# Kernel tuning notes

Measured on AMD Instinct MI355X. Metric: run time of the kernel, lower is better.

## Reference

```python
import jax, jax.numpy as jnp
import numpy as np

N, E, D, LM, NF, M = 512, 16384, 1280, 1024, 256, 64

def setup_inputs() -> dict:
    key = jax.random.key(0)
    ks = jax.random.split(key, 10)
    lm_embedding = jax.random.normal(ks[0], (1, N + 2, LM), jnp.float32)
    node_feat = jax.random.normal(ks[1], (N, NF), jnp.float32)
    edge_feat = jax.random.uniform(ks[2], (E, 1), jnp.float32)
    src = jax.random.randint(ks[3], (E,), 0, N)
    dst = jax.random.randint(ks[4], (E,), 0, N)
    mask_index = jax.random.randint(ks[5], (M,), 0, N)
    W_g = jax.random.normal(ks[6], (D, D), jnp.float32) / np.sqrt(D).astype(np.float32)
    b_g = jnp.zeros((D,), jnp.float32)
    W_d = jax.random.normal(ks[7], (D, 1), jnp.float32) / np.sqrt(D).astype(np.float32)
    b_d = jnp.zeros((1,), jnp.float32)
    W_m = jax.random.normal(ks[8], (D, 2), jnp.float32) / np.sqrt(D).astype(np.float32)
    b_m = jnp.zeros((2,), jnp.float32)
    return {"lm_embedding": lm_embedding, "node_feat": node_feat, "edge_feat": edge_feat,
            "src": src, "dst": dst, "mask_index": mask_index,
            "W_g": W_g, "b_g": b_g, "W_d": W_d, "b_d": b_d, "W_m": W_m, "b_m": b_m}

def reference(lm_embedding, node_feat, edge_feat, src, dst, mask_index,
              W_g, b_g, W_d, b_d, W_m, b_m):
    # concat LM embedding (strip BOS/EOS) with structural features -> (N, D)
    h = jnp.concatenate([lm_embedding[0, 1:-1, :], node_feat], axis=1)
    # GINConv('max'): messages = h[src] * edge_weight, max-reduce onto dst
    msg = h[src] * edge_feat                                   # (E, D)
    neigh = jax.ops.segment_max(msg, dst, num_segments=h.shape[0])
    neigh = jnp.where(jnp.isneginf(neigh), 0.0, neigh)         # isolated nodes -> 0 (DGL semantics)
    rst = (h + neigh) @ W_g + b_g                              # (1+eps)*h + neigh, eps=0, then Linear
    node_output = rst + h                                      # residual
    # dis_pred[i, j] = sigmoid(W_d . (h_j - h_i) + b_d); collapse to per-node projection
    p = (node_output @ W_d)[:, 0]                              # (N,)
    dis_pred = jax.nn.sigmoid(p[None, :] - p[:, None] + b_d[0])[..., None]  # (N, N, 1)
    mask_pred = jnp.tanh(node_output[mask_index] @ W_m + b_m)  # (M, 2)
    return (dis_pred, mask_pred)
```

## Files before the change

### kernel.cpp

```cpp
#include <hip/hip_runtime.h>
#include <float.h>
#include <math.h>

#define N 512
#define E 16384
#define D 1280
#define LMDIM 1024
#define NFDIM 256
#define M 64
#define MAXDEG 512

#define WPROJ_BLOCKS 161
#define BIN_BLOCKS 32

__device__ __forceinline__ float4 h_vec4(const float* __restrict__ lm,
                                         const float* __restrict__ nf,
                                         int i, int t) {
  return (t < 256) ? *(const float4*)&lm[(size_t)(i + 1) * LMDIM + t * 4]
                   : *(const float4*)&nf[(size_t)i * NFDIM + (t - 256) * 4];
}

__device__ __forceinline__ float wred(float v) {
#pragma unroll
  for (int off = 32; off > 0; off >>= 1) v += __shfl_xor(v, off, 64);
  return v;
}

__global__ __launch_bounds__(512) void prep_kernel(
    const float* __restrict__ Wg, const float* __restrict__ Wd,
    const float* __restrict__ Wm, const float* __restrict__ bg,
    const int* __restrict__ src, const int* __restrict__ dst,
    const float* __restrict__ ew,
    float* __restrict__ wd2, float* __restrict__ wm2,
    float* __restrict__ consts,
    int* __restrict__ cnt, int2* __restrict__ bin) {
  const int b = blockIdx.x;
  const int t = threadIdx.x;
  if (b < WPROJ_BLOCKS) {
    const int wid = t >> 6, lane = t & 63;
    const int r = b * 8 + wid;
    if (r > D) return;
    const float* row = (r < D) ? &Wg[(size_t)r * D] : bg;
    float d0 = 0.f, d1 = 0.f, d2 = 0.f;
#pragma unroll
    for (int k = 0; k < 5; ++k) {
      int u = lane + 64 * k;
      float4 wv = *(const float4*)&row[u * 4];
      float4 vd = *(const float4*)&Wd[u * 4];
      d0 += wv.x * vd.x + wv.y * vd.y + wv.z * vd.z + wv.w * vd.w;
      float4 m01 = *(const float4*)&Wm[u * 8];
      float4 m23 = *(const float4*)&Wm[u * 8 + 4];
      d1 += wv.x * m01.x + wv.y * m01.z + wv.z * m23.x + wv.w * m23.z;
      d2 += wv.x * m01.y + wv.y * m01.w + wv.z * m23.y + wv.w * m23.w;
    }
    d0 = wred(d0); d1 = wred(d1); d2 = wred(d2);
    if (lane == 0) {
      if (r < D) {
        wd2[r] = d0; wm2[2 * r] = d1; wm2[2 * r + 1] = d2;
      } else {
        consts[0] = d0; consts[1] = d1; consts[2] = d2;
      }
    }
  } else {
    const int e = (b - WPROJ_BLOCKS) * 512 + t;
    int d = dst[e];
    int pos = atomicAdd(&cnt[d], 1);
    if (pos < MAXDEG)
      bin[(size_t)d * MAXDEG + pos] = make_int2(src[e], __float_as_int(ew[e]));
  }
}

__global__ __launch_bounds__(320) void neighp_kernel(
    const float* __restrict__ lm, const float* __restrict__ nf,
    const int* __restrict__ mask_index,
    const float* __restrict__ Wd, const float* __restrict__ Wm,
    const float* __restrict__ bm,
    const float* __restrict__ wd2, const float* __restrict__ wm2,
    const float* __restrict__ consts,
    const int* __restrict__ cnt_g, const int2* __restrict__ bin,
    float* __restrict__ p, float* __restrict__ out) {
  __shared__ int   s_src[MAXDEG];
  __shared__ float s_w[MAXDEG];
  __shared__ float r0s[5], r1s[5], r2s[5];
  __shared__ float s_m1, s_m2;

  const int n = blockIdx.x;
  const int t = threadIdx.x;
  const int wid = t >> 6, lane = t & 63;

  const int cnt = min(cnt_g[n], MAXDEG);
  for (int i = t; i < cnt; i += 320) {
    int2 pe = bin[(size_t)n * MAXDEG + i];
    s_src[i] = pe.x;
    s_w[i] = __int_as_float(pe.y);
  }
  __syncthreads();

  float4 m = make_float4(-FLT_MAX, -FLT_MAX, -FLT_MAX, -FLT_MAX);
  int i = 0;
  for (; i + 8 <= cnt; i += 8) {
    float4 v[8];
    float wgt[8];
#pragma unroll
    for (int j = 0; j < 8; ++j) {
      int s = s_src[i + j];
      wgt[j] = s_w[i + j];
      v[j] = h_vec4(lm, nf, s, t);
    }
#pragma unroll
    for (int j = 0; j < 8; ++j) {
      m.x = fmaxf(m.x, v[j].x * wgt[j]);
      m.y = fmaxf(m.y, v[j].y * wgt[j]);
      m.z = fmaxf(m.z, v[j].z * wgt[j]);
      m.w = fmaxf(m.w, v[j].w * wgt[j]);
    }
  }
  for (; i < cnt; ++i) {
    int s = s_src[i];
    float wgt = s_w[i];
    float4 v = h_vec4(lm, nf, s, t);
    m.x = fmaxf(m.x, v.x * wgt);
    m.y = fmaxf(m.y, v.y * wgt);
    m.z = fmaxf(m.z, v.z * wgt);
    m.w = fmaxf(m.w, v.w * wgt);
  }
  const bool has = (cnt > 0);
  float4 hv = h_vec4(lm, nf, n, t);
  float4 a;
  a.x = hv.x + (has ? m.x : 0.0f);
  a.y = hv.y + (has ? m.y : 0.0f);
  a.z = hv.z + (has ? m.z : 0.0f);
  a.w = hv.w + (has ? m.w : 0.0f);

  float4 w2 = *(const float4*)&wd2[t * 4];
  float4 vd = *(const float4*)&Wd[t * 4];
  float pd = a.x * w2.x + a.y * w2.y + a.z * w2.z + a.w * w2.w
           + hv.x * vd.x + hv.y * vd.y + hv.z * vd.z + hv.w * vd.w;
  float4 q01 = *(const float4*)&wm2[t * 8];
  float4 q23 = *(const float4*)&wm2[t * 8 + 4];
  float4 m01 = *(const float4*)&Wm[t * 8];
  float4 m23 = *(const float4*)&Wm[t * 8 + 4];
  float a0 = a.x * q01.x + a.y * q01.z + a.z * q23.x + a.w * q23.z
           + hv.x * m01.x + hv.y * m01.z + hv.z * m23.x + hv.w * m23.z;
  float a1 = a.x * q01.y + a.y * q01.w + a.z * q23.y + a.w * q23.w
           + hv.x * m01.y + hv.y * m01.w + hv.z * m23.y + hv.w * m23.w;

  pd = wred(pd); a0 = wred(a0); a1 = wred(a1);
  if (lane == 0) { r0s[wid] = pd; r1s[wid] = a0; r2s[wid] = a1; }
  __syncthreads();
  if (t == 0) {
    p[n] = r0s[0] + r0s[1] + r0s[2] + r0s[3] + r0s[4] + consts[0];
    s_m1 = r1s[0] + r1s[1] + r1s[2] + r1s[3] + r1s[4] + consts[1];
    s_m2 = r2s[0] + r2s[1] + r2s[2] + r2s[3] + r2s[4] + consts[2];
  }
  __syncthreads();
  if (t < M && mask_index[t] == n) {
    out[(size_t)N * N + t * 2 + 0] = tanhf(s_m1 + bm[0]);
    out[(size_t)N * N + t * 2 + 1] = tanhf(s_m2 + bm[1]);
  }
}

__global__ __launch_bounds__(256) void dis_kernel(const float* __restrict__ p,
                                                  const float* __restrict__ bd,
                                                  float* __restrict__ out) {
  int b = blockIdx.x;
  int t = threadIdx.x;
  int i = b * 2 + (t >> 7);
  int j4 = (t & 127) * 4;
  float pi = p[i];
  float bias = bd[0];
  float4 pj = *(const float4*)&p[j4];
  float4 o;
  o.x = 1.0f / (1.0f + __expf(-(pj.x - pi + bias)));
  o.y = 1.0f / (1.0f + __expf(-(pj.y - pi + bias)));
  o.z = 1.0f / (1.0f + __expf(-(pj.z - pi + bias)));
  o.w = 1.0f / (1.0f + __expf(-(pj.w - pi + bias)));
  *(float4*)&out[(size_t)i * N + j4] = o;
}


extern "C" void kernel_launch(void* const* d_in, const int* in_sizes, int n_in,
                              void* d_out, int out_size, void* d_ws, size_t ws_size,
                              hipStream_t stream) {
  const float* lm = (const float*)d_in[0];
  const float* nf = (const float*)d_in[1];
  const float* ew = (const float*)d_in[2];
  const int* src = (const int*)d_in[3];
  const int* dst = (const int*)d_in[4];
  const int* mask_index = (const int*)d_in[5];
  const float* Wg = (const float*)d_in[6];
  const float* bg = (const float*)d_in[7];
  const float* Wd = (const float*)d_in[8];
  const float* bd = (const float*)d_in[9];
  const float* Wm = (const float*)d_in[10];
  const float* bm = (const float*)d_in[11];
  float* out = (float*)d_out;
  char* w = (char*)d_ws;

  int2*  bin    = (int2*)(w);
  int*   cnt    = (int*)(w + 2097152);
  float* wd2    = (float*)(w + 2099200);
  float* wm2    = (float*)(w + 2104320);
  float* consts = (float*)(w + 2114560);
  float* p      = (float*)(w + 2114576);

  hipMemsetAsync(cnt, 0, N * sizeof(int), stream);
  prep_kernel<<<WPROJ_BLOCKS + BIN_BLOCKS, 512, 0, stream>>>(
      Wg, Wd, Wm, bg, src, dst, ew, wd2, wm2, consts, cnt, bin);
  neighp_kernel<<<N, 320, 0, stream>>>(lm, nf, mask_index, Wd, Wm, bm,
                                       wd2, wm2, consts, cnt, bin, p, out);
  dis_kernel<<<N / 2, 256, 0, stream>>>(p, bd, out);
}
```

Baseline: 98.91 us.

## Replace global atomic edge binning with per-block dst scan in shared memory

Drops the memset and the global atomic bucketing of edges by destination. Each node block now scans the whole dst array itself and collects its matching edge indices with shared-memory atomics, then gathers src and edge weights. This removes one launch, the memset and the global atomic traffic. In exchange every one of the 512 blocks reads all 64KB of dst from cache, and neighbour order inside a bin becomes nondeterministic, which does not matter for a max reduction.

Result: no change. 97.98 us (-0.9%).

```diff
diff --git a/kernel.cpp b/kernel.cpp
--- a/kernel.cpp
+++ b/kernel.cpp
@@ -11,7 +11,6 @@
 #define MAXDEG 512
 
 #define WPROJ_BLOCKS 161
-#define BIN_BLOCKS 32
 
 __device__ __forceinline__ float4 h_vec4(const float* __restrict__ lm,
                                          const float* __restrict__ nf,
@@ -26,73 +25,73 @@
   return v;
 }
 
-__global__ __launch_bounds__(512) void prep_kernel(
+__global__ __launch_bounds__(512) void wproj_kernel(
     const float* __restrict__ Wg, const float* __restrict__ Wd,
     const float* __restrict__ Wm, const float* __restrict__ bg,
-    const int* __restrict__ src, const int* __restrict__ dst,
-    const float* __restrict__ ew,
     float* __restrict__ wd2, float* __restrict__ wm2,
-    float* __restrict__ consts,
-    int* __restrict__ cnt, int2* __restrict__ bin) {
-  const int b = blockIdx.x;
-  const int t = threadIdx.x;
-  if (b < WPROJ_BLOCKS) {
-    const int wid = t >> 6, lane = t & 63;
-    const int r = b * 8 + wid;
-    if (r > D) return;
-    const float* row = (r < D) ? &Wg[(size_t)r * D] : bg;
-    float d0 = 0.f, d1 = 0.f, d2 = 0.f;
-#pragma unroll
-    for (int k = 0; k < 5; ++k) {
-      int u = lane + 64 * k;
-      float4 wv = *(const float4*)&row[u * 4];
-      float4 vd = *(const float4*)&Wd[u * 4];
-      d0 += wv.x * vd.x + wv.y * vd.y + wv.z * vd.z + wv.w * vd.w;
-      float4 m01 = *(const float4*)&Wm[u * 8];
-      float4 m23 = *(const float4*)&Wm[u * 8 + 4];
-      d1 += wv.x * m01.x + wv.y * m01.z + wv.z * m23.x + wv.w * m23.z;
-      d2 += wv.x * m01.y + wv.y * m01.w + wv.z * m23.y + wv.w * m23.w;
+    float* __restrict__ consts) {
+  const int wid = threadIdx.x >> 6, lane = threadIdx.x & 63;
+  const int r = blockIdx.x * 8 + wid;
+  if (r > D) return;
+  const float* row = (r < D) ? &Wg[(size_t)r * D] : bg;
+  float d0 = 0.f, d1 = 0.f, d2 = 0.f;
+#pragma unroll
+  for (int k = 0; k < 5; ++k) {
+    int u = lane + 64 * k;
+    float4 wv = *(const float4*)&row[u * 4];
+    float4 vd = *(const float4*)&Wd[u * 4];
+    d0 += wv.x * vd.x + wv.y * vd.y + wv.z * vd.z + wv.w * vd.w;
+    float4 m01 = *(const float4*)&Wm[u * 8];
+    float4 m23 = *(const float4*)&Wm[u * 8 + 4];
+    d1 += wv.x * m01.x + wv.y * m01.z + wv.z * m23.x + wv.w * m23.z;
+    d2 += wv.x * m01.y + wv.y * m01.w + wv.z * m23.y + wv.w * m23.w;
+  }
+  d0 = wred(d0); d1 = wred(d1); d2 = wred(d2);
+  if (lane == 0) {
+    if (r < D) {
+      wd2[r] = d0; wm2[2 * r] = d1; wm2[2 * r + 1] = d2;
+    } else {
+      consts[0] = d0; consts[1] = d1; consts[2] = d2;
     }
-    d0 = wred(d0); d1 = wred(d1); d2 = wred(d2);
-    if (lane == 0) {
-      if (r < D) {
-        wd2[r] = d0; wm2[2 * r] = d1; wm2[2 * r + 1] = d2;
-      } else {
-        consts[0] = d0; consts[1] = d1; consts[2] = d2;
-      }
-    }
-  } else {
-    const int e = (b - WPROJ_BLOCKS) * 512 + t;
-    int d = dst[e];
-    int pos = atomicAdd(&cnt[d], 1);
-    if (pos < MAXDEG)
-      bin[(size_t)d * MAXDEG + pos] = make_int2(src[e], __float_as_int(ew[e]));
   }
 }
 
 __global__ __launch_bounds__(320) void neighp_kernel(
     const float* __restrict__ lm, const float* __restrict__ nf,
-    const int* __restrict__ mask_index,
+    const float* __restrict__ ew, const int* __restrict__ src,
+    const int* __restrict__ dst, const int* __restrict__ mask_index,
     const float* __restrict__ Wd, const float* __restrict__ Wm,
     const float* __restrict__ bm,
     const float* __restrict__ wd2, const float* __restrict__ wm2,
     const float* __restrict__ consts,
-    const int* __restrict__ cnt_g, const int2* __restrict__ bin,
     float* __restrict__ p, float* __restrict__ out) {
+  __shared__ int   s_e[MAXDEG];
   __shared__ int   s_src[MAXDEG];
   __shared__ float s_w[MAXDEG];
+  __shared__ int   s_cnt;
   __shared__ float r0s[5], r1s[5], r2s[5];
   __shared__ float s_m1, s_m2;
 
   const int n = blockIdx.x;
   const int t = threadIdx.x;
   const int wid = t >> 6, lane = t & 63;
-
-  const int cnt = min(cnt_g[n], MAXDEG);
+  if (t == 0) s_cnt = 0;
+  __syncthreads();
+
+  const int4* dst4 = (const int4*)dst;
+  for (int i = t; i < E / 4; i += 320) {
+    int4 d4 = dst4[i];
+    if (d4.x == n) { int pos = atomicAdd(&s_cnt, 1); if (pos < MAXDEG) s_e[pos] = 4 * i + 0; }
+    if (d4.y == n) { int pos = atomicAdd(&s_cnt, 1); if (pos < MAXDEG) s_e[pos] = 4 * i + 1; }
+    if (d4.z == n) { int pos = atomicAdd(&s_cnt, 1); if (pos < MAXDEG) s_e[pos] = 4 * i + 2; }
+    if (d4.w == n) { int pos = atomicAdd(&s_cnt, 1); if (pos < MAXDEG) s_e[pos] = 4 * i + 3; }
+  }
+  __syncthreads();
+  const int cnt = min(s_cnt, MAXDEG);
   for (int i = t; i < cnt; i += 320) {
-    int2 pe = bin[(size_t)n * MAXDEG + i];
-    s_src[i] = pe.x;
-    s_w[i] = __int_as_float(pe.y);
+    int e = s_e[i];
+    s_src[i] = src[e];
+    s_w[i] = ew[e];
   }
   __syncthreads();
 
@@ -197,17 +196,13 @@
   float* out = (float*)d_out;
   char* w = (char*)d_ws;
 
-  int2*  bin    = (int2*)(w);
-  int*   cnt    = (int*)(w + 2097152);
-  float* wd2    = (float*)(w + 2099200);
-  float* wm2    = (float*)(w + 2104320);
-  float* consts = (float*)(w + 2114560);
-  float* p      = (float*)(w + 2114576);
-
-  hipMemsetAsync(cnt, 0, N * sizeof(int), stream);
-  prep_kernel<<<WPROJ_BLOCKS + BIN_BLOCKS, 512, 0, stream>>>(
-      Wg, Wd, Wm, bg, src, dst, ew, wd2, wm2, consts, cnt, bin);
-  neighp_kernel<<<N, 320, 0, stream>>>(lm, nf, mask_index, Wd, Wm, bm,
-                                       wd2, wm2, consts, cnt, bin, p, out);
+  float* wd2    = (float*)(w);
+  float* wm2    = (float*)(w + 5120);
+  float* consts = (float*)(w + 15360);
+  float* p      = (float*)(w + 15488);
+
+  wproj_kernel<<<WPROJ_BLOCKS, 512, 0, stream>>>(Wg, Wd, Wm, bg, wd2, wm2, consts);
+  neighp_kernel<<<N, 320, 0, stream>>>(lm, nf, ew, src, dst, mask_index,
+                                       Wd, Wm, bm, wd2, wm2, consts, p, out);
   dis_kernel<<<N / 2, 256, 0, stream>>>(p, bd, out);
 }
```
